# Kernel optimization log

Measured on AMD Instinct MI355X. Metric: run time of the kernel, lower is better.

The kernel has to match this reference:

```python
import jax, jax.numpy as jnp
import numpy as np

D = 64        # d_model = input_dims
S = 300       # patch_length
DFF = 256     # dff (H feature dim)
NH = 2        # num_heads
DK = D // NH  # 32


def _ln(x, g, b, eps=1e-5):
    m = x.mean(-1, keepdims=True)
    v = ((x - m) ** 2).mean(-1, keepdims=True)
    return (x - m) * jax.lax.rsqrt(v + eps) * g + b


def setup_inputs() -> dict:
    key = jax.random.key(0)
    ks = jax.random.split(key, 20)
    B = 256
    inp = {
        "state": jax.random.normal(ks[0], (B, S, D), dtype=jnp.float32),
        "H": jax.random.normal(ks[1], (B, S, DFF), dtype=jnp.float32),
    }
    # Linear weights stored as [in, out] (torch stores [out, in]; math is x @ W_in_out + b)
    def lin(k, din, dout):
        k1, k2 = jax.random.split(k)
        w = jax.random.normal(k1, (din, dout), dtype=jnp.float32) / np.sqrt(din)
        b = jax.random.normal(k2, (dout,), dtype=jnp.float32) * 0.01
        return w, b
    inp["Wq"], inp["bq"] = lin(ks[2], D, D)
    inp["Wk"], inp["bk"] = lin(ks[3], D, D)
    inp["Wv"], inp["bv"] = lin(ks[4], D, D)
    inp["Wcq"], inp["bcq"] = lin(ks[5], DFF, D)
    inp["Wck"], inp["bck"] = lin(ks[6], DFF, D)
    inp["Wcv"], inp["bcv"] = lin(ks[7], DFF, D)
    # six LayerNorms on d_model (QE/KE/VE from state branch, QH/KH/VH from H branch)
    for name in ["QE", "KE", "VE", "QH", "KH", "VH"]:
        inp[f"g{name}"] = jnp.ones((D,), jnp.float32)
        inp[f"beta{name}"] = jnp.zeros((D,), jnp.float32)
    inp["W1"], inp["b1"] = lin(ks[8], D, 4 * D)
    inp["W2"], inp["b2"] = lin(ks[9], 4 * D, D)
    inp["g1"] = jnp.ones((D,), jnp.float32)   # norm1
    inp["beta1"] = jnp.zeros((D,), jnp.float32)
    return inp


def reference(state, H, Wq, bq, Wk, bk, Wv, bv, Wcq, bcq, Wck, bck, Wcv, bcv,
              gQE, betaQE, gKE, betaKE, gVE, betaVE,
              gQH, betaQH, gKH, betaKH, gVH, betaVH,
              W1, b1, W2, b2, g1, beta1):
    B = state.shape[0]
    # gated q/k/v: LN(Linear(state)) * LN(Linear(H)), split into heads
    def branch(Wx, bx, gx, bbx, Wh, bh, gh, bbh):
        e = _ln(state @ Wx + bx, gx, bbx)
        h = _ln(H @ Wh + bh, gh, bbh)
        return (e * h).reshape(B, S, NH, DK).transpose(0, 2, 1, 3)  # [B,NH,S,DK]
    q = branch(Wq, bq, gQE, betaQE, Wcq, bcq, gQH, betaQH)
    k = branch(Wk, bk, gKE, betaKE, Wck, bck, gKH, betaKH)
    v = branch(Wv, bv, gVE, betaVE, Wcv, bcv, gVH, betaVH)
    scores = jnp.einsum("bhqd,bhkd->bhqk", q, k) / jnp.sqrt(jnp.float32(DK))
    attn = jax.nn.softmax(scores, axis=-1)
    out = jnp.einsum("bhqk,bhkd->bhqd", attn, v)
    out = out.transpose(0, 2, 1, 3).reshape(B, S, NH * DK)
    Z1 = state + out                      # dropout p=0.01 -> identity in eval
    Z2 = _ln(Z1, g1, beta1)
    Z3 = jax.nn.gelu(Z2 @ W1 + b1, approximate=False)  # torch F.gelu default = exact erf
    Z4 = Z3 @ W2 + b2
    return Z1 + Z4
```

## Files before the change

### kernel.cpp

```cpp
#include <hip/hip_runtime.h>
#include <math.h>

namespace {

constexpr int SEQ  = 300;
constexpr int DM   = 64;
constexpr int DFFN = 256;
constexpr int NBAT = 256;
constexpr int ROWS = NBAT * SEQ;
constexpr float EPS = 1e-5f;

typedef __attribute__((ext_vector_type(8))) short s16x8;
typedef __attribute__((ext_vector_type(4))) float f32x4;

__device__ __forceinline__ float4 ld4(const float* p) { return *reinterpret_cast<const float4*>(p); }

__device__ __forceinline__ ushort f2bf(float x) {
  unsigned u = __builtin_bit_cast(unsigned, x);
  u += 0x7FFFu + ((u >> 16) & 1u);
  return (ushort)(u >> 16);
}

struct PrepArgs {
  const float *Wq,*Wk,*Wv,*Wcq,*Wck,*Wcv;
  const float *bq,*bk,*bv,*bcq,*bck,*bcv;
  const float *gQE,*betaQE,*gKE,*betaKE,*gVE,*betaVE;
  const float *gQH,*betaQH,*gKH,*betaKH,*gVH,*betaVH;
  const float *W1,*W2;
  ushort *Bqkv, *W1t, *W2t;
  float *pk;
};

__global__ __launch_bounds__(256) void tb_prep(PrepArgs P) {
  const int idx = blockIdx.x * 256 + threadIdx.x;
  if (idx < 61440) {
    const int c = idx / 12288, rem = idx % 12288;
    const int n = rem >> 6, k = rem & 63;
    const int br = n >> 6, col = n & 63;
    float v;
    if (c == 0) {
      const float* W = (br == 0) ? P.Wq : (br == 1) ? P.Wk : P.Wv;
      v = W[k * DM + col];
    } else {
      const float* W = (br == 0) ? P.Wcq : (br == 1) ? P.Wck : P.Wcv;
      v = W[((c - 1) * 64 + k) * DM + col];
    }
    P.Bqkv[c * 12288 + ((n * 128 + ((k * 2) ^ ((n & 7) << 4))) >> 1)] = f2bf(v);
  } else if (idx < 77824) {
    const int r = idx - 61440, n = r >> 6, k = r & 63;
    P.W1t[(n * 128 + ((k * 2) ^ ((n & 7) << 4))) >> 1] = f2bf(P.W1[k * DFFN + n]);
  } else if (idx < 94208) {
    const int j = idx - 77824;
    const int fragId = j >> 9, within = j & 511;
    const int lane = within >> 3, e = within & 7;
    const int ps = fragId >> 2, nt2 = fragId & 3;
    const int n = nt2 * 16 + (lane & 15);
    const int k = ps * 32 + ((e >> 2) << 4) + ((lane >> 4) << 2) + (e & 3);
    P.W2t[j] = f2bf(P.W2[k * DM + n]);
  } else if (idx < 95360) {
    const int r = idx - 94208, which = r / 192, j = r % 192;
    const int br = j >> 6, col = j & 63;
    const float* s;
    switch (which) {
      case 0:  s = (br==0)?P.bq   :(br==1)?P.bk    :P.bv;     break;
      case 1:  s = (br==0)?P.bcq  :(br==1)?P.bck   :P.bcv;    break;
      case 2:  s = (br==0)?P.gQE  :(br==1)?P.gKE   :P.gVE;    break;
      case 3:  s = (br==0)?P.betaQE:(br==1)?P.betaKE:P.betaVE; break;
      case 4:  s = (br==0)?P.gQH  :(br==1)?P.gKH   :P.gVH;    break;
      default: s = (br==0)?P.betaQH:(br==1)?P.betaKH:P.betaVH; break;
    }
    P.pk[which * 192 + j] = s[col];
  }
}

struct QkvArgs {
  const float *state, *H;
  const ushort *Bqkv;
  const float *pk;
  ushort *qo, *ko, *vo;
};

__global__ __launch_bounds__(256) void tb_qkv(QkvArgs A) {
  __shared__ __align__(16) ushort Ab[4608];
  __shared__ __align__(16) ushort Bb[12288];
  const int t = threadIdx.x;
  const int lane = t & 63, w = t >> 6;
  const int lo = lane & 15, hi = lane >> 4;
  const int rowbase = blockIdx.x * 64;

  f32x4 accE[12], accH[12];
  #pragma unroll
  for (int nt = 0; nt < 12; ++nt) {
    const float bE = A.pk[nt * 16 + lo], bH = A.pk[192 + nt * 16 + lo];
    accE[nt] = (f32x4){bE, bE, bE, bE};
    accH[nt] = (f32x4){bH, bH, bH, bH};
  }

  const int arow = w * 16 + lo;
  const int aswz = (lo & 7) << 4;

#define STAGE_B(c)                                                            \
  _Pragma("unroll")                                                           \
  for (int i = 0; i < 6; ++i) {                                               \
    const int s_ = i * 256 + t;                                               \
    *(uint4*)&Bb[s_ * 8] = *(const uint4*)&A.Bqkv[(c) * 12288 + s_ * 8];      \
  }

#define STAGE_A(SRC, STRIDE)                                                  \
  _Pragma("unroll")                                                           \
  for (int i = 0; i < 4; ++i) {                                               \
    const int p_ = i * 256 + t;                                               \
    const int row_ = p_ >> 4, slot_ = p_ & 15;                                \
    const float4 f_ = ld4(&(SRC)[row_ * (STRIDE) + slot_ * 4]);               \
    ushort4 u_;                                                               \
    u_.x = f2bf(f_.x); u_.y = f2bf(f_.y); u_.z = f2bf(f_.z); u_.w = f2bf(f_.w);\
    *(ushort4*)((char*)Ab + (row_ * 128 + ((slot_ * 8) ^ ((row_ & 7) << 4)))) = u_; \
  }

#define COMPUTE(ACC)                                                          \
  _Pragma("unroll")                                                           \
  for (int ks = 0; ks < 2; ++ks) {                                            \
    const s16x8 af = *(const s16x8*)((const char*)Ab +                        \
        (arow * 128 + ((ks * 64 + hi * 16) ^ aswz)));                         \
    _Pragma("unroll")                                                         \
    for (int nt = 0; nt < 12; ++nt) {                                         \
      const int n_ = nt * 16 + lo;                                            \
      const s16x8 bf = *(const s16x8*)((const char*)Bb +                      \
          (n_ * 128 + ((ks * 64 + hi * 16) ^ ((n_ & 7) << 4))));              \
      ACC[nt] = __builtin_amdgcn_mfma_f32_16x16x32_bf16(af, bf, ACC[nt], 0, 0, 0); \
    }                                                                         \
  }

  STAGE_B(0)
  STAGE_A(A.state + (size_t)rowbase * 64, 64)
  __syncthreads();
  COMPUTE(accE)
  for (int c = 1; c < 5; ++c) {
    __syncthreads();
    STAGE_B(c)
    const float* hsrc = A.H + (size_t)rowbase * 256 + (c - 1) * 64;
    STAGE_A(hsrc, 256)
    __syncthreads();
    COMPUTE(accH)
  }
#undef STAGE_B
#undef STAGE_A
#undef COMPUTE

  const float* gE  = A.pk + 384;
  const float* bEt = A.pk + 576;
  const float* gH  = A.pk + 768;
  const float* bHt = A.pk + 960;
  const int growbase = rowbase + w * 16 + hi * 4;
  float vout[4][4];

  #pragma unroll
  for (int br = 0; br < 3; ++br) {
    #pragma unroll
    for (int r = 0; r < 4; ++r) {
      float s1 = 0.f, s2 = 0.f, u1 = 0.f, u2 = 0.f;
      #pragma unroll
      for (int qq = 0; qq < 4; ++qq) {
        const float ev = accE[br * 4 + qq][r], hv = accH[br * 4 + qq][r];
        s1 += ev; s2 += ev * ev; u1 += hv; u2 += hv * hv;
      }
      #pragma unroll
      for (int m = 1; m <= 8; m <<= 1) {
        s1 += __shfl_xor(s1, m, 64); s2 += __shfl_xor(s2, m, 64);
        u1 += __shfl_xor(u1, m, 64); u2 += __shfl_xor(u2, m, 64);
      }
      const float me = s1 * (1.f / 64.f);
      const float re = rsqrtf(s2 * (1.f / 64.f) - me * me + EPS);
      const float mh = u1 * (1.f / 64.f);
      const float rh = rsqrtf(u2 * (1.f / 64.f) - mh * mh + EPS);
      const int grow = growbase + r;
      const int bb = grow / 300, ss = grow - bb * 300;
      #pragma unroll
      for (int qq = 0; qq < 4; ++qq) {
        const int colg = (br * 4 + qq) * 16 + lo;
        const float en = (accE[br * 4 + qq][r] - me) * re * gE[colg] + bEt[colg];
        const float hn = (accH[br * 4 + qq][r] - mh) * rh * gH[colg] + bHt[colg];
        const float val = en * hn;
        if (br == 2) {
          vout[r][qq] = val;
        } else {
          const int cb = qq * 16 + lo;
          const int hh = cb >> 5, dk = cb & 31;
          ushort* dst = (br == 0) ? A.qo : A.ko;
          const float sc = (br == 0) ? 0.17677669529663687f : 1.f;
          dst[((size_t)(bb * 2 + hh) * 300 + ss) * 32 + dk] = f2bf(val * sc);
        }
      }
    }
  }

  __syncthreads();
  ushort* vbuf = Ab;
  #pragma unroll
  for (int r = 0; r < 4; ++r) {
    const int sl = w * 16 + hi * 4 + r;
    #pragma unroll
    for (int qq = 0; qq < 4; ++qq) {
      const int dk = qq * 16 + lo;
      vbuf[dk * 68 + sl] = f2bf(vout[r][qq]);
    }
  }
  __syncthreads();
  #pragma unroll
  for (int i = 0; i < 4; ++i) {
    const int p = i * 256 + t;
    const int dk = p >> 4, sg = p & 15;
    const int grow = rowbase + sg * 4;
    const int bb = grow / 300, ss = grow - bb * 300;
    const int hh = dk >> 5, dkh = dk & 31;
    ushort4 val;
    val.x = vbuf[dk * 68 + sg * 4 + 0];
    val.y = vbuf[dk * 68 + sg * 4 + 1];
    val.z = vbuf[dk * 68 + sg * 4 + 2];
    val.w = vbuf[dk * 68 + sg * 4 + 3];
    *(ushort4*)&A.vo[(size_t)(bb * 2 + hh) * 9600 + dkh * 300 + ss] = val;
  }
}

__global__ __launch_bounds__(256, 2) void tb_attn(const ushort* __restrict__ q,
    const ushort* __restrict__ k, const ushort* __restrict__ vt, float* __restrict__ ao)
{
  __shared__ __align__(16) char lq[304 * 64];
  __shared__ __align__(16) char lk[304 * 64];
  __shared__ __align__(16) char lv[32 * 656];

  const int t = threadIdx.x;
  const int hh = blockIdx.x, b = blockIdx.y;
  const size_t bh = (size_t)(b * 2 + hh);

  const char* qg = (const char*)(q + bh * 300 * 32);
  const char* kg = (const char*)(k + bh * 300 * 32);
  const char* vg = (const char*)(vt + bh * 32 * 300);

  for (int c = t; c < 1216; c += 256) {
    const int lin = c * 16;
    const int row = c >> 2;
    uint4 val = make_uint4(0u, 0u, 0u, 0u);
    if (row < 300) val = *(const uint4*)(qg + lin);
    *(uint4*)(lq + (lin ^ ((lin >> 2) & 0x70))) = val;
  }
  for (int c = t; c < 1216; c += 256) {
    const int lin = c * 16;
    const int row = c >> 2;
    uint4 val = make_uint4(0u, 0u, 0u, 0u);
    if (row < 300) val = *(const uint4*)(kg + lin);
    *(uint4*)(lk + (lin ^ ((lin >> 2) & 0x70))) = val;
  }
  for (int i = t; i < 320; i += 256) {
    const int row = i / 10, cc = i - row * 10;
    *(unsigned*)(lv + row * 656 + 600 + cc * 4) = 0u;
  }
  for (int i = t; i < 2400; i += 256) {
    const int row = i / 75, cc = i - row * 75;
    *(uint2*)(lv + row * 656 + cc * 8) = *(const uint2*)(vg + row * 600 + cc * 8);
  }
  __syncthreads();

  const int lane = t & 63, wid = t >> 6;
  const int lo = lane & 15, hi = lane >> 4;
  const f32x4 zero = {0.f, 0.f, 0.f, 0.f};

  for (int qt = wid; qt < 19; qt += 4) {
    int qa = (qt * 16 + lo) * 64 + hi * 16;
    qa ^= (qa >> 2) & 0x70;
    const s16x8 qf = *(const s16x8*)(lq + qa);

    f32x4 p[19];
    #pragma unroll
    for (int kt = 0; kt < 19; ++kt) {
      int ka = (kt * 16 + lo) * 64 + hi * 16;
      ka ^= (ka >> 2) & 0x70;
      const s16x8 kf = *(const s16x8*)(lk + ka);
      p[kt] = __builtin_amdgcn_mfma_f32_16x16x32_bf16(kf, qf, zero, 0, 0, 0);
    }

    float mx = -1e30f;
    #pragma unroll
    for (int kt = 0; kt < 19; ++kt)
      #pragma unroll
      for (int r = 0; r < 4; ++r) mx = fmaxf(mx, p[kt][r]);
    mx = fmaxf(mx, __shfl_xor(mx, 16, 64));
    mx = fmaxf(mx, __shfl_xor(mx, 32, 64));

    #pragma unroll
    for (int kt = 0; kt < 19; ++kt)
      #pragma unroll
      for (int r = 0; r < 4; ++r) p[kt][r] = __expf(p[kt][r] - mx);
    if (hi == 3) p[18] = zero;

    float sum = 0.f;
    #pragma unroll
    for (int kt = 0; kt < 19; ++kt)
      #pragma unroll
      for (int r = 0; r < 4; ++r) sum += p[kt][r];
    sum += __shfl_xor(sum, 16, 64);
    sum += __shfl_xor(sum, 32, 64);
    const float inv = 1.f / sum;

    s16x8 pb[10];
    #pragma unroll
    for (int pr = 0; pr < 9; ++pr) {
      uint4 wv;
      wv.x = (unsigned)f2bf(p[2*pr][0] * inv)   | ((unsigned)f2bf(p[2*pr][1] * inv) << 16);
      wv.y = (unsigned)f2bf(p[2*pr][2] * inv)   | ((unsigned)f2bf(p[2*pr][3] * inv) << 16);
      wv.z = (unsigned)f2bf(p[2*pr+1][0] * inv) | ((unsigned)f2bf(p[2*pr+1][1] * inv) << 16);
      wv.w = (unsigned)f2bf(p[2*pr+1][2] * inv) | ((unsigned)f2bf(p[2*pr+1][3] * inv) << 16);
      pb[pr] = __builtin_bit_cast(s16x8, wv);
    }
    {
      uint4 wv;
      wv.x = (unsigned)f2bf(p[18][0] * inv) | ((unsigned)f2bf(p[18][1] * inv) << 16);
      wv.y = (unsigned)f2bf(p[18][2] * inv) | ((unsigned)f2bf(p[18][3] * inv) << 16);
      wv.z = 0u; wv.w = 0u;
      pb[9] = __builtin_bit_cast(s16x8, wv);
    }

    f32x4 acc0 = zero, acc1 = zero;
    #pragma unroll
    for (int pr = 0; pr < 10; ++pr) {
      const int byte0 = pr * 64 + hi * 8;
      uint4 w0, w1;
      {
        const uint2 a = *(const uint2*)(lv + lo * 656 + byte0);
        const uint2 c = *(const uint2*)(lv + lo * 656 + byte0 + 32);
        w0.x = a.x; w0.y = a.y; w0.z = c.x; w0.w = c.y;
      }
      {
        const uint2 a = *(const uint2*)(lv + (lo + 16) * 656 + byte0);
        const uint2 c = *(const uint2*)(lv + (lo + 16) * 656 + byte0 + 32);
        w1.x = a.x; w1.y = a.y; w1.z = c.x; w1.w = c.y;
      }
      acc0 = __builtin_amdgcn_mfma_f32_16x16x32_bf16(pb[pr], __builtin_bit_cast(s16x8, w0), acc0, 0, 0, 0);
      acc1 = __builtin_amdgcn_mfma_f32_16x16x32_bf16(pb[pr], __builtin_bit_cast(s16x8, w1), acc1, 0, 0, 0);
    }

    float* aop = ao + ((size_t)b * 300) * 64 + hh * 32;
    const int s0 = qt * 16 + hi * 4;
    #pragma unroll
    for (int r = 0; r < 4; ++r) {
      const int s = s0 + r;
      if (s < 300) {
        aop[s * 64 + lo]      = acc0[r];
        aop[s * 64 + 16 + lo] = acc1[r];
      }
    }
  }
}

struct FfnArgs {
  const float *state, *ao;
  const ushort *W1t, *W2t;
  const float *b1, *b2, *g1, *beta1;
  float* out;
};

__global__ __launch_bounds__(256) void tb_ffn(FfnArgs F) {
  __shared__ __align__(16) ushort Z2b[4096];
  __shared__ __align__(16) ushort Wb[16384];
  const int t = threadIdx.x;
  const int lane = t & 63, w = t >> 6;
  const int lo = lane & 15, hi = lane >> 4;
  const int rowbase = blockIdx.x * 64;

  #pragma unroll
  for (int i = 0; i < 8; ++i) {
    const int s_ = i * 256 + t;
    *(uint4*)&Wb[s_ * 8] = *(const uint4*)&F.W1t[s_ * 8];
  }

  {
    const int lrow = t >> 2;
    const int lcg  = (t & 3) * 16;
    const size_t gb = (size_t)(rowbase + lrow) * 64 + lcg;
    float xv[16];
    #pragma unroll
    for (int i = 0; i < 4; ++i) {
      const float4 a = ld4(&F.state[gb + i * 4]);
      const float4 b = ld4(&F.ao[gb + i * 4]);
      xv[i*4+0] = a.x + b.x; xv[i*4+1] = a.y + b.y;
      xv[i*4+2] = a.z + b.z; xv[i*4+3] = a.w + b.w;
    }
    float s1 = 0.f, s2 = 0.f;
    #pragma unroll
    for (int j = 0; j < 16; ++j) { s1 += xv[j]; s2 += xv[j] * xv[j]; }
    s1 += __shfl_xor(s1, 1, 64); s2 += __shfl_xor(s2, 1, 64);
    s1 += __shfl_xor(s1, 2, 64); s2 += __shfl_xor(s2, 2, 64);
    const float mean = s1 * (1.f / 64.f);
    const float rstd = rsqrtf(s2 * (1.f / 64.f) - mean * mean + EPS);
    float gv[16], bv[16];
    #pragma unroll
    for (int i = 0; i < 4; ++i) {
      *(float4*)&gv[i*4] = ld4(&F.g1[lcg + i * 4]);
      *(float4*)&bv[i*4] = ld4(&F.beta1[lcg + i * 4]);
    }
    #pragma unroll
    for (int h = 0; h < 2; ++h) {
      float z[8];
      #pragma unroll
      for (int j = 0; j < 8; ++j)
        z[j] = (xv[h*8+j] - mean) * rstd * gv[h*8+j] + bv[h*8+j];
      uint4 pkd;
      pkd.x = (unsigned)f2bf(z[0]) | ((unsigned)f2bf(z[1]) << 16);
      pkd.y = (unsigned)f2bf(z[2]) | ((unsigned)f2bf(z[3]) << 16);
      pkd.z = (unsigned)f2bf(z[4]) | ((unsigned)f2bf(z[5]) << 16);
      pkd.w = (unsigned)f2bf(z[6]) | ((unsigned)f2bf(z[7]) << 16);
      *(uint4*)((char*)Z2b + (lrow * 128 + (((lcg + h * 8) * 2) ^ ((lrow & 7) << 4)))) = pkd;
    }
  }
  __syncthreads();

  const int arow = w * 16 + lo;
  const int aswz = (lo & 7) << 4;

  s16x8 zf0, zf1;
  zf0 = *(const s16x8*)((const char*)Z2b + (arow * 128 + ((0 * 64 + hi * 16) ^ aswz)));
  zf1 = *(const s16x8*)((const char*)Z2b + (arow * 128 + ((1 * 64 + hi * 16) ^ aswz)));

  s16x8 pz[8];
  #pragma unroll
  for (int ps = 0; ps < 8; ++ps) {
    const int n0 = (2 * ps) * 16, n1 = (2 * ps + 1) * 16;
    const float4 bb0 = ld4(&F.b1[n0 + hi * 4]);
    const float4 bb1 = ld4(&F.b1[n1 + hi * 4]);
    f32x4 a0 = (f32x4){bb0.x, bb0.y, bb0.z, bb0.w};
    f32x4 a1 = (f32x4){bb1.x, bb1.y, bb1.z, bb1.w};
    #pragma unroll
    for (int ks = 0; ks < 2; ++ks) {
      const s16x8 zf = ks ? zf1 : zf0;
      const int na = n0 + lo, nb = n1 + lo;
      const s16x8 wfa = *(const s16x8*)((const char*)Wb + (na * 128 + ((ks * 64 + hi * 16) ^ ((na & 7) << 4))));
      const s16x8 wfb = *(const s16x8*)((const char*)Wb + (nb * 128 + ((ks * 64 + hi * 16) ^ ((nb & 7) << 4))));
      a0 = __builtin_amdgcn_mfma_f32_16x16x32_bf16(wfa, zf, a0, 0, 0, 0);
      a1 = __builtin_amdgcn_mfma_f32_16x16x32_bf16(wfb, zf, a1, 0, 0, 0);
    }
    float ga[8];
    #pragma unroll
    for (int e = 0; e < 8; ++e) {
      const float xg = (e < 4) ? a0[e & 3] : a1[e & 3];
      ga[e] = 0.5f * xg * (1.f + erff(xg * 0.70710678118654752f));
    }
    uint4 wv;
    wv.x = (unsigned)f2bf(ga[0]) | ((unsigned)f2bf(ga[1]) << 16);
    wv.y = (unsigned)f2bf(ga[2]) | ((unsigned)f2bf(ga[3]) << 16);
    wv.z = (unsigned)f2bf(ga[4]) | ((unsigned)f2bf(ga[5]) << 16);
    wv.w = (unsigned)f2bf(ga[6]) | ((unsigned)f2bf(ga[7]) << 16);
    pz[ps] = __builtin_bit_cast(s16x8, wv);
  }
  __syncthreads();

  #pragma unroll
  for (int i = 0; i < 8; ++i) {
    const int s_ = i * 256 + t;
    *(uint4*)&Wb[s_ * 8] = *(const uint4*)&F.W2t[s_ * 8];
  }
  __syncthreads();

  f32x4 acc2[4];
  #pragma unroll
  for (int nt = 0; nt < 4; ++nt) { const float b = F.b2[nt * 16 + lo]; acc2[nt] = (f32x4){b, b, b, b}; }
  #pragma unroll
  for (int ps = 0; ps < 8; ++ps) {
    #pragma unroll
    for (int nt = 0; nt < 4; ++nt) {
      const s16x8 bf = *(const s16x8*)&Wb[((ps * 4 + nt) * 64 + lane) * 8];
      acc2[nt] = __builtin_amdgcn_mfma_f32_16x16x32_bf16(pz[ps], bf, acc2[nt], 0, 0, 0);
    }
  }

  #pragma unroll
  for (int nt = 0; nt < 4; ++nt) {
    #pragma unroll
    for (int r = 0; r < 4; ++r) {
      const int grow = rowbase + w * 16 + hi * 4 + r;
      const int col = nt * 16 + lo;
      const size_t gidx = (size_t)grow * 64 + col;
      const float z1 = F.state[gidx] + F.ao[gidx];
      F.out[gidx] = z1 + acc2[nt][r];
    }
  }
}

}

extern "C" void kernel_launch(void* const* d_in, const int* in_sizes, int n_in,
                              void* d_out, int out_size, void* d_ws, size_t ws_size,
                              hipStream_t stream)
{
  const float* state = (const float*)d_in[0];
  const float* H     = (const float*)d_in[1];
  const float* Wq  = (const float*)d_in[2];  const float* bq  = (const float*)d_in[3];
  const float* Wk  = (const float*)d_in[4];  const float* bk  = (const float*)d_in[5];
  const float* Wv  = (const float*)d_in[6];  const float* bv  = (const float*)d_in[7];
  const float* Wcq = (const float*)d_in[8];  const float* bcq = (const float*)d_in[9];
  const float* Wck = (const float*)d_in[10]; const float* bck = (const float*)d_in[11];
  const float* Wcv = (const float*)d_in[12]; const float* bcv = (const float*)d_in[13];
  const float* gQE = (const float*)d_in[14]; const float* betaQE = (const float*)d_in[15];
  const float* gKE = (const float*)d_in[16]; const float* betaKE = (const float*)d_in[17];
  const float* gVE = (const float*)d_in[18]; const float* betaVE = (const float*)d_in[19];
  const float* gQH = (const float*)d_in[20]; const float* betaQH = (const float*)d_in[21];
  const float* gKH = (const float*)d_in[22]; const float* betaKH = (const float*)d_in[23];
  const float* gVH = (const float*)d_in[24]; const float* betaVH = (const float*)d_in[25];
  const float* W1 = (const float*)d_in[26]; const float* b1 = (const float*)d_in[27];
  const float* W2 = (const float*)d_in[28]; const float* b2 = (const float*)d_in[29];
  const float* g1 = (const float*)d_in[30]; const float* beta1 = (const float*)d_in[31];

  constexpr size_t QKV_E = (size_t)NBAT * 2 * 300 * 32;
  float*  ao_ws = (float*)d_ws;
  ushort* q_ws  = (ushort*)(ao_ws + (size_t)ROWS * DM);
  ushort* k_ws  = q_ws + QKV_E;
  ushort* v_ws  = k_ws + QKV_E;
  ushort* Bqkv  = v_ws + QKV_E;
  ushort* W1t   = Bqkv + 61440;
  ushort* W2t   = W1t + 16384;
  float*  pk    = (float*)(W2t + 16384);

  PrepArgs P;
  P.Wq = Wq; P.Wk = Wk; P.Wv = Wv; P.Wcq = Wcq; P.Wck = Wck; P.Wcv = Wcv;
  P.bq = bq; P.bk = bk; P.bv = bv; P.bcq = bcq; P.bck = bck; P.bcv = bcv;
  P.gQE = gQE; P.betaQE = betaQE; P.gKE = gKE; P.betaKE = betaKE;
  P.gVE = gVE; P.betaVE = betaVE; P.gQH = gQH; P.betaQH = betaQH;
  P.gKH = gKH; P.betaKH = betaKH; P.gVH = gVH; P.betaVH = betaVH;
  P.W1 = W1; P.W2 = W2;
  P.Bqkv = Bqkv; P.W1t = W1t; P.W2t = W2t; P.pk = pk;
  tb_prep<<<373, 256, 0, stream>>>(P);

  QkvArgs A;
  A.state = state; A.H = H; A.Bqkv = Bqkv; A.pk = pk;
  A.qo = q_ws; A.ko = k_ws; A.vo = v_ws;
  tb_qkv<<<ROWS / 64, 256, 0, stream>>>(A);

  tb_attn<<<dim3(2, NBAT), 256, 0, stream>>>(q_ws, k_ws, v_ws, ao_ws);

  FfnArgs F;
  F.state = state; F.ao = ao_ws; F.W1t = W1t; F.W2t = W2t;
  F.b1 = b1; F.b2 = b2; F.g1 = g1; F.beta1 = beta1; F.out = (float*)d_out;
  tb_ffn<<<ROWS / 64, 256, 0, stream>>>(F);
}
```

Before: 127.0 us.

## Prefetch next QKV chunk into registers during MFMA and stage q/k stores via LDS

The qkv projection kernel now issues global loads for the next H chunk and weight chunk into registers before computing the current chunk, then writes them to shared memory after compute, so global latency overlaps with MFMA work. It also stages the q and k outputs through shared memory so they go out as vectorized ushort4 stores instead of scattered 2-byte writes. The cost is more registers for the prefetch buffers and a larger combined shared buffer, which may reduce occupancy.

```diff
diff --git a/kernel.cpp b/kernel.cpp
--- a/kernel.cpp
+++ b/kernel.cpp
@@ -81,8 +81,9 @@
 };
 
 __global__ __launch_bounds__(256) void tb_qkv(QkvArgs A) {
-  __shared__ __align__(16) ushort Ab[4608];
-  __shared__ __align__(16) ushort Bb[12288];
+  __shared__ __align__(16) ushort sh[20480];
+  ushort* Ab = sh;
+  ushort* Bb = sh + 8192;
   const int t = threadIdx.x;
   const int lane = t & 63, w = t >> 6;
   const int lo = lane & 15, hi = lane >> 4;
@@ -98,24 +99,6 @@
 
   const int arow = w * 16 + lo;
   const int aswz = (lo & 7) << 4;
-
-#define STAGE_B(c)                                                            \
-  _Pragma("unroll")                                                           \
-  for (int i = 0; i < 6; ++i) {                                               \
-    const int s_ = i * 256 + t;                                               \
-    *(uint4*)&Bb[s_ * 8] = *(const uint4*)&A.Bqkv[(c) * 12288 + s_ * 8];      \
-  }
-
-#define STAGE_A(SRC, STRIDE)                                                  \
-  _Pragma("unroll")                                                           \
-  for (int i = 0; i < 4; ++i) {                                               \
-    const int p_ = i * 256 + t;                                               \
-    const int row_ = p_ >> 4, slot_ = p_ & 15;                                \
-    const float4 f_ = ld4(&(SRC)[row_ * (STRIDE) + slot_ * 4]);               \
-    ushort4 u_;                                                               \
-    u_.x = f2bf(f_.x); u_.y = f2bf(f_.y); u_.z = f2bf(f_.z); u_.w = f2bf(f_.w);\
-    *(ushort4*)((char*)Ab + (row_ * 128 + ((slot_ * 8) ^ ((row_ & 7) << 4)))) = u_; \
-  }
 
 #define COMPUTE(ACC)                                                          \
   _Pragma("unroll")                                                           \
@@ -131,28 +114,72 @@
     }                                                                         \
   }
 
-  STAGE_B(0)
-  STAGE_A(A.state + (size_t)rowbase * 64, 64)
+  #pragma unroll
+  for (int i = 0; i < 6; ++i) {
+    const int s_ = i * 256 + t;
+    *(uint4*)&Bb[s_ * 8] = *(const uint4*)&A.Bqkv[s_ * 8];
+  }
+  {
+    const float* src = A.state + (size_t)rowbase * 64;
+    #pragma unroll
+    for (int i = 0; i < 4; ++i) {
+      const int p = i * 256 + t;
+      const int row_ = p >> 4, slot_ = p & 15;
+      const float4 f_ = ld4(&src[row_ * 64 + slot_ * 4]);
+      ushort4 u_;
+      u_.x = f2bf(f_.x); u_.y = f2bf(f_.y); u_.z = f2bf(f_.z); u_.w = f2bf(f_.w);
+      *(ushort4*)((char*)Ab + (row_ * 128 + ((slot_ * 8) ^ ((row_ & 7) << 4)))) = u_;
+    }
+  }
   __syncthreads();
-  COMPUTE(accE)
-  for (int c = 1; c < 5; ++c) {
+
+  #pragma unroll 1
+  for (int c = 0; c < 5; ++c) {
+    float4 apre[4];
+    uint4  bpre[6];
+    if (c < 4) {
+      const float* hsrc = A.H + (size_t)rowbase * 256 + c * 64;
+      #pragma unroll
+      for (int i = 0; i < 4; ++i) {
+        const int p = i * 256 + t;
+        apre[i] = ld4(&hsrc[(p >> 4) * 256 + (p & 15) * 4]);
+      }
+      #pragma unroll
+      for (int i = 0; i < 6; ++i) {
+        const int s_ = i * 256 + t;
+        bpre[i] = *(const uint4*)&A.Bqkv[(size_t)(c + 1) * 12288 + s_ * 8];
+      }
+    }
+    if (c == 0) { COMPUTE(accE) } else { COMPUTE(accH) }
     __syncthreads();
-    STAGE_B(c)
-    const float* hsrc = A.H + (size_t)rowbase * 256 + (c - 1) * 64;
-    STAGE_A(hsrc, 256)
-    __syncthreads();
-    COMPUTE(accH)
-  }
-#undef STAGE_B
-#undef STAGE_A
+    if (c < 4) {
+      #pragma unroll
+      for (int i = 0; i < 6; ++i) {
+        const int s_ = i * 256 + t;
+        *(uint4*)&Bb[s_ * 8] = bpre[i];
+      }
+      #pragma unroll
+      for (int i = 0; i < 4; ++i) {
+        const int p = i * 256 + t;
+        const int row_ = p >> 4, slot_ = p & 15;
+        ushort4 u_;
+        u_.x = f2bf(apre[i].x); u_.y = f2bf(apre[i].y);
+        u_.z = f2bf(apre[i].z); u_.w = f2bf(apre[i].w);
+        *(ushort4*)((char*)Ab + (row_ * 128 + ((slot_ * 8) ^ ((row_ & 7) << 4)))) = u_;
+      }
+      __syncthreads();
+    }
+  }
 #undef COMPUTE
 
+  ushort* vq = sh;
+  ushort* vk = sh + 4352;
+  ushort* vv = sh + 8704;
   const float* gE  = A.pk + 384;
   const float* bEt = A.pk + 576;
   const float* gH  = A.pk + 768;
   const float* bHt = A.pk + 960;
-  const int growbase = rowbase + w * 16 + hi * 4;
-  float vout[4][4];
+  const int lrow0 = w * 16 + hi * 4;
 
   #pragma unroll
   for (int br = 0; br < 3; ++br) {
@@ -173,52 +200,48 @@
       const float re = rsqrtf(s2 * (1.f / 64.f) - me * me + EPS);
       const float mh = u1 * (1.f / 64.f);
       const float rh = rsqrtf(u2 * (1.f / 64.f) - mh * mh + EPS);
-      const int grow = growbase + r;
-      const int bb = grow / 300, ss = grow - bb * 300;
       #pragma unroll
       for (int qq = 0; qq < 4; ++qq) {
         const int colg = (br * 4 + qq) * 16 + lo;
         const float en = (accE[br * 4 + qq][r] - me) * re * gE[colg] + bEt[colg];
         const float hn = (accH[br * 4 + qq][r] - mh) * rh * gH[colg] + bHt[colg];
         const float val = en * hn;
-        if (br == 2) {
-          vout[r][qq] = val;
-        } else {
-          const int cb = qq * 16 + lo;
-          const int hh = cb >> 5, dk = cb & 31;
-          ushort* dst = (br == 0) ? A.qo : A.ko;
-          const float sc = (br == 0) ? 0.17677669529663687f : 1.f;
-          dst[((size_t)(bb * 2 + hh) * 300 + ss) * 32 + dk] = f2bf(val * sc);
-        }
-      }
-    }
-  }
-
+        const int cb = qq * 16 + lo;
+        if (br == 0)      vq[(lrow0 + r) * 68 + cb] = f2bf(val * 0.17677669529663687f);
+        else if (br == 1) vk[(lrow0 + r) * 68 + cb] = f2bf(val);
+        else              vv[cb * 68 + (lrow0 + r)] = f2bf(val);
+      }
+    }
+  }
   __syncthreads();
-  ushort* vbuf = Ab;
-  #pragma unroll
-  for (int r = 0; r < 4; ++r) {
-    const int sl = w * 16 + hi * 4 + r;
-    #pragma unroll
-    for (int qq = 0; qq < 4; ++qq) {
-      const int dk = qq * 16 + lo;
-      vbuf[dk * 68 + sl] = f2bf(vout[r][qq]);
-    }
-  }
-  __syncthreads();
+
+  #pragma unroll
+  for (int br = 0; br < 2; ++br) {
+    ushort* dst = br ? A.ko : A.qo;
+    const ushort* src = br ? vk : vq;
+    #pragma unroll
+    for (int i = 0; i < 4; ++i) {
+      const int g = i * 256 + t;
+      const int row = g >> 4, c4 = (g & 15) * 4;
+      const int grow = rowbase + row, bb = grow / 300, ss = grow - bb * 300;
+      const int hh2 = c4 >> 5, dkh = c4 & 31;
+      *(ushort4*)&dst[((size_t)(bb * 2 + hh2) * 300 + ss) * 32 + dkh] =
+          *(const ushort4*)&src[row * 68 + c4];
+    }
+  }
   #pragma unroll
   for (int i = 0; i < 4; ++i) {
     const int p = i * 256 + t;
     const int dk = p >> 4, sg = p & 15;
     const int grow = rowbase + sg * 4;
     const int bb = grow / 300, ss = grow - bb * 300;
-    const int hh = dk >> 5, dkh = dk & 31;
+    const int hh2 = dk >> 5, dkh = dk & 31;
     ushort4 val;
-    val.x = vbuf[dk * 68 + sg * 4 + 0];
-    val.y = vbuf[dk * 68 + sg * 4 + 1];
-    val.z = vbuf[dk * 68 + sg * 4 + 2];
-    val.w = vbuf[dk * 68 + sg * 4 + 3];
-    *(ushort4*)&A.vo[(size_t)(bb * 2 + hh) * 9600 + dkh * 300 + ss] = val;
+    val.x = vv[dk * 68 + sg * 4 + 0];
+    val.y = vv[dk * 68 + sg * 4 + 1];
+    val.z = vv[dk * 68 + sg * 4 + 2];
+    val.w = vv[dk * 68 + sg * 4 + 3];
+    *(ushort4*)&A.vo[(size_t)(bb * 2 + hh2) * 9600 + dkh * 300 + ss] = val;
   }
 }
 
```

After: 175.9 us. +38.5%, slower.
